# Kernel tuning notes

Measured on AMD Instinct MI355X. Metric: run time of the kernel, lower is better.

The kernel has to match this reference:

```python
import jax, jax.numpy as jnp
import numpy as np

B, N_IN, D_IN = 2048, 49, 320
D = 768            # inner_dim
H = 8              # n_heads
DH = D // H        # head dim = 96
NQ = 8             # n_queries
D_OUT = 3072       # llama_hidden
EPS = 1e-5


def _ln(x, g, b):
    mu = jnp.mean(x, axis=-1, keepdims=True)
    var = jnp.mean(jnp.square(x - mu), axis=-1, keepdims=True)
    return (x - mu) * jax.lax.rsqrt(var + EPS) * g + b


def setup_inputs() -> dict:
    key = jax.random.key(0)
    ks = jax.random.split(key, 16)
    s = lambda k, shape, fan: jax.random.normal(k, shape, jnp.float32) * (1.0 / np.sqrt(fan))
    return {
        "features": jax.random.normal(ks[0], (B, N_IN, D_IN), jnp.float32),
        "input_proj_w": s(ks[1], (D, D_IN), D_IN),
        "input_proj_b": jnp.zeros((D,), jnp.float32),
        "queries": jax.random.normal(ks[2], (NQ, D), jnp.float32) * 0.02,
        "ln_q_g": jnp.ones((D,), jnp.float32), "ln_q_b": jnp.zeros((D,), jnp.float32),
        "ln_kv_g": jnp.ones((D,), jnp.float32), "ln_kv_b": jnp.zeros((D,), jnp.float32),
        "in_proj_w": s(ks[3], (3 * D, D), D),
        "in_proj_b": jnp.zeros((3 * D,), jnp.float32),
        "out_proj_w": s(ks[4], (D, D), D),
        "out_proj_b": jnp.zeros((D,), jnp.float32),
        "ln_ff_g": jnp.ones((D,), jnp.float32), "ln_ff_b": jnp.zeros((D,), jnp.float32),
        "ffn_w1": s(ks[5], (D, D), D), "ffn_b1": jnp.zeros((D,), jnp.float32),
        "ffn_w2": s(ks[6], (D, D), D), "ffn_b2": jnp.zeros((D,), jnp.float32),
        "output_proj_w": s(ks[7], (D_OUT, D), D),
        "output_proj_b": jnp.zeros((D_OUT,), jnp.float32),
        "final_g": jnp.ones((D_OUT,), jnp.float32), "final_b": jnp.zeros((D_OUT,), jnp.float32),
    }


def reference(features, input_proj_w, input_proj_b, queries,
              ln_q_g, ln_q_b, ln_kv_g, ln_kv_b,
              in_proj_w, in_proj_b, out_proj_w, out_proj_b,
              ln_ff_g, ln_ff_b, ffn_w1, ffn_b1, ffn_w2, ffn_b2,
              output_proj_w, output_proj_b, final_g, final_b):
    b = features.shape[0]
    # kv projection: (B, N_in, D)
    kv = jnp.einsum('bnd,ed->bne', features, input_proj_w) + input_proj_b
    q = jnp.broadcast_to(queries[None], (b, NQ, D))

    # --- single layer (n_layers=1) ---
    q_norm = _ln(q, ln_q_g, ln_q_b)
    kv_norm = _ln(kv, ln_kv_g, ln_kv_b)

    wq, wk, wv = in_proj_w[:D], in_proj_w[D:2 * D], in_proj_w[2 * D:]
    bq, bk, bv = in_proj_b[:D], in_proj_b[D:2 * D], in_proj_b[2 * D:]
    qp = (jnp.einsum('bqd,ed->bqe', q_norm, wq) + bq).reshape(b, NQ, H, DH)
    kp = (jnp.einsum('bnd,ed->bne', kv_norm, wk) + bk).reshape(b, N_IN, H, DH)
    vp = (jnp.einsum('bnd,ed->bne', kv_norm, wv) + bv).reshape(b, N_IN, H, DH)

    scores = jnp.einsum('bqhd,bnhd->bhqn', qp, kp) / np.sqrt(DH).astype(np.float32)
    attn = jax.nn.softmax(scores, axis=-1)
    ctx = jnp.einsum('bhqn,bnhd->bqhd', attn, vp).reshape(b, NQ, D)
    attn_out = jnp.einsum('bqd,ed->bqe', ctx, out_proj_w) + out_proj_b

    q = q + attn_out
    h = _ln(q, ln_ff_g, ln_ff_b)
    h = jnp.einsum('bqd,ed->bqe', h, ffn_w1) + ffn_b1
    h = jax.nn.gelu(h, approximate=False)
    h = jnp.einsum('bqd,ed->bqe', h, ffn_w2) + ffn_b2
    q = q + h

    out = jnp.einsum('bqd,ed->bqe', q, output_proj_w) + output_proj_b
    return _ln(out, final_g, final_b)
```

## Files before the change

kernel.cpp:

```cpp
#include <hip/hip_runtime.h>
#include <math.h>

typedef __attribute__((ext_vector_type(8))) short short8;
typedef __attribute__((ext_vector_type(8))) unsigned short ushort8;
typedef __attribute__((ext_vector_type(4))) float f32x4;

__device__ __forceinline__ float b2f(unsigned short h) {
    union { unsigned int u; float f; } c; c.u = ((unsigned int)h) << 16; return c.f;
}
__device__ __forceinline__ unsigned short f2b(float x) {
    union { float f; unsigned int u; } c; c.f = x;
    unsigned int r = c.u + 0x7fffu + ((c.u >> 16) & 1u);
    return (unsigned short)(r >> 16);
}

__global__ __launch_bounds__(256) void cast_f2b(const float* __restrict__ in,
                                                unsigned short* __restrict__ out, int n4) {
    int i = blockIdx.x * 256 + threadIdx.x;
    if (i >= n4) return;
    float4 f = ((const float4*)in)[i];
    ushort4 o; o.x = f2b(f.x); o.y = f2b(f.y); o.z = f2b(f.z); o.w = f2b(f.w);
    ((ushort4*)out)[i] = o;
}

template <int DD, bool INB, bool OUTB>
__global__ __launch_bounds__(256) void ln_rows(const void* __restrict__ in_, void* __restrict__ out_,
                                               const float* __restrict__ g, const float* __restrict__ bb,
                                               int nrows) {
    const int wv = threadIdx.x >> 6, l = threadIdx.x & 63;
    const int row = blockIdx.x * 4 + wv;
    if (row >= nrows) return;
    constexpr int NC = DD / 256;
    float v[DD / 64];
    if constexpr (INB) {
        const ushort4* in = (const ushort4*)((const unsigned short*)in_ + (size_t)row * DD);
#pragma unroll
        for (int c = 0; c < NC; ++c) {
            ushort4 u = in[l + 64 * c];
            v[4*c] = b2f(u.x); v[4*c+1] = b2f(u.y); v[4*c+2] = b2f(u.z); v[4*c+3] = b2f(u.w);
        }
    } else {
        const float4* in = (const float4*)((const float*)in_ + (size_t)row * DD);
#pragma unroll
        for (int c = 0; c < NC; ++c) {
            float4 u = in[l + 64 * c];
            v[4*c] = u.x; v[4*c+1] = u.y; v[4*c+2] = u.z; v[4*c+3] = u.w;
        }
    }
    float s = 0.f, s2 = 0.f;
#pragma unroll
    for (int i = 0; i < DD / 64; ++i) { s += v[i]; s2 += v[i] * v[i]; }
#pragma unroll
    for (int o = 32; o > 0; o >>= 1) { s += __shfl_xor(s, o, 64); s2 += __shfl_xor(s2, o, 64); }
    const float mu = s * (1.0f / DD);
    const float var = s2 * (1.0f / DD) - mu * mu;
    const float rs = rsqrtf(var + 1e-5f);
    if constexpr (OUTB) {
        ushort4* out = (ushort4*)((unsigned short*)out_ + (size_t)row * DD);
#pragma unroll
        for (int c = 0; c < NC; ++c) {
            int e = (l + 64 * c) * 4;
            ushort4 o4;
            o4.x = f2b((v[4*c]   - mu) * rs * g[e]   + bb[e]);
            o4.y = f2b((v[4*c+1] - mu) * rs * g[e+1] + bb[e+1]);
            o4.z = f2b((v[4*c+2] - mu) * rs * g[e+2] + bb[e+2]);
            o4.w = f2b((v[4*c+3] - mu) * rs * g[e+3] + bb[e+3]);
            out[l + 64 * c] = o4;
        }
    } else {
        float4* out = (float4*)((float*)out_ + (size_t)row * DD);
#pragma unroll
        for (int c = 0; c < NC; ++c) {
            int e = (l + 64 * c) * 4;
            float4 o4;
            o4.x = (v[4*c]   - mu) * rs * g[e]   + bb[e];
            o4.y = (v[4*c+1] - mu) * rs * g[e+1] + bb[e+1];
            o4.z = (v[4*c+2] - mu) * rs * g[e+2] + bb[e+2];
            o4.w = (v[4*c+3] - mu) * rs * g[e+3] + bb[e+3];
            out[l + 64 * c] = o4;
        }
    }
}

__global__ __launch_bounds__(256) void ln_stats(const unsigned short* __restrict__ kv,
                                                float2* __restrict__ stats, int nrows) {
    const int wv = threadIdx.x >> 6, l = threadIdx.x & 63;
    const int row = blockIdx.x * 4 + wv;
    if (row >= nrows) return;
    const ushort4* in = (const ushort4*)(kv + (size_t)row * 768);
    float s = 0.f, s2 = 0.f;
#pragma unroll
    for (int c = 0; c < 3; ++c) {
        ushort4 u = in[l + 64 * c];
        float a = b2f(u.x), b = b2f(u.y), cc = b2f(u.z), d = b2f(u.w);
        s += a + b + cc + d;
        s2 += a * a + b * b + cc * cc + d * d;
    }
#pragma unroll
    for (int o = 32; o > 0; o >>= 1) { s += __shfl_xor(s, o, 64); s2 += __shfl_xor(s2, o, 64); }
    const float mu = s * (1.0f / 768.0f);
    const float var = s2 * (1.0f / 768.0f) - mu * mu;
    const float rs = rsqrtf(var + 1e-5f);
    if (l == 0) stats[row] = make_float2(rs, rs * mu);
}

__global__ __launch_bounds__(256) void qp_kernel(const float* __restrict__ qn, const float* __restrict__ wq,
                                                 const float* __restrict__ bq, float* __restrict__ qp) {
    int q = blockIdx.x / 3;
    int col = (blockIdx.x % 3) * 256 + threadIdx.x;
    const float4* a = (const float4*)(qn + q * 768);
    const float4* wr = (const float4*)(wq + (size_t)col * 768);
    float s = 0.f;
#pragma unroll 8
    for (int k = 0; k < 192; ++k) {
        float4 xx = a[k], yy = wr[k];
        s += xx.x * yy.x + xx.y * yy.y + xx.z * yy.z + xx.w * yy.w;
    }
    qp[q * 768 + col] = s + bq[col];
}

__global__ __launch_bounds__(256) void qk_build(const float* __restrict__ qp, const float* __restrict__ wk,
                                                const float* __restrict__ g,
                                                unsigned short* __restrict__ qkg, float* __restrict__ tout) {
    __shared__ float red[4];
    const int hq = blockIdx.x, h = hq >> 3, q = hq & 7;
    const int tid = threadIdx.x;
    const float* qv = qp + q * 768 + h * 96;
    float tsum = 0.f;
#pragma unroll
    for (int c = 0; c < 3; ++c) {
        int e = tid + 256 * c;
        float s = 0.f;
        for (int d = 0; d < 96; ++d) s += qv[d] * wk[(size_t)(h * 96 + d) * 768 + e];
        unsigned short bv = f2b(s * 0.10206207262f * g[e]);
        qkg[hq * 768 + e] = bv;
        tsum += b2f(bv);
    }
#pragma unroll
    for (int o = 32; o > 0; o >>= 1) tsum += __shfl_xor(tsum, o, 64);
    if ((tid & 63) == 0) red[tid >> 6] = tsum;
    __syncthreads();
    if (tid == 0) tout[hq] = red[0] + red[1] + red[2] + red[3];
}

__device__ __forceinline__ void gll16(const void* g, void* l) {
    __builtin_amdgcn_global_load_lds((const __attribute__((address_space(1))) unsigned int*)g,
                                     (__attribute__((address_space(3))) unsigned int*)l, 16, 0, 0);
}

template <int ROWS>
__device__ __forceinline__ void stage_rows(const unsigned short* gbase, int ldg,
                                           unsigned short* lds, int tid) {
    int wuni = tid & ~63;
#pragma unroll
    for (int it = 0; it < ROWS / 32; ++it) {
        int s = it * 256 + tid;
        int r = s >> 3, c = s & 7;
        int cc = c ^ (r & 7);
        gll16(gbase + (size_t)r * ldg + cc * 8, lds + (size_t)(it * 256 + wuni) * 8);
    }
}

template <int EPI>
__global__ __launch_bounds__(256) void gemm_bf16(
    const unsigned short* __restrict__ A, const unsigned short* __restrict__ W,
    const float* __restrict__ bias, void* __restrict__ out,
    const float* __restrict__ aux, int K, int N) {
    __shared__ __align__(16) unsigned short lA[128 * 64];
    __shared__ __align__(16) unsigned short lB[128 * 64];
    const int tid = threadIdx.x;
    const int l = tid & 63, w = tid >> 6;
    int gx = gridDim.x;
    int lid = blockIdx.y * gx + blockIdx.x;
    int nwg = gx * gridDim.y;
    int idx = (nwg & 7) ? lid : ((lid & 7) * (nwg >> 3) + (lid >> 3));
    const int bm0 = (idx / gx) * 128, bn0 = (idx % gx) * 128;
    const int wm = (w >> 1) * 64, wn = (w & 1) * 64;
    const int l15 = l & 15, lk = l >> 4;
    f32x4 acc[4][4] = {};
    const int nk = K >> 6;
    const unsigned short* Abase = A + (size_t)bm0 * K;
    const unsigned short* Wbase = W + (size_t)bn0 * K;
    for (int kt = 0; kt < nk; ++kt) {
        stage_rows<128>(Abase + kt * 64, K, lA, tid);
        stage_rows<128>(Wbase + kt * 64, K, lB, tid);
        __syncthreads();
        short8 af[4], bf[4];
#pragma unroll
        for (int kk = 0; kk < 2; ++kk) {
#pragma unroll
            for (int mf = 0; mf < 4; ++mf) {
                int r = wm + mf * 16 + l15;
                int c = (kk * 4 + lk) ^ (r & 7);
                af[mf] = *(const short8*)(lA + r * 64 + c * 8);
            }
#pragma unroll
            for (int nf = 0; nf < 4; ++nf) {
                int r = wn + nf * 16 + l15;
                int c = (kk * 4 + lk) ^ (r & 7);
                bf[nf] = *(const short8*)(lB + r * 64 + c * 8);
            }
#pragma unroll
            for (int mf = 0; mf < 4; ++mf)
#pragma unroll
                for (int nf = 0; nf < 4; ++nf)
                    acc[mf][nf] = __builtin_amdgcn_mfma_f32_16x16x32_bf16(af[mf], bf[nf], acc[mf][nf], 0, 0, 0);
        }
        __syncthreads();
    }
    const int row0 = bm0 + wm + (lk << 2);
    const int col0 = bn0 + wn + l15;
#pragma unroll
    for (int nf = 0; nf < 4; ++nf) {
        int col = col0 + nf * 16;
        float bv = bias[col];
#pragma unroll
        for (int mf = 0; mf < 4; ++mf) {
#pragma unroll
            for (int r = 0; r < 4; ++r) {
                int row = row0 + mf * 16 + r;
                float v = acc[mf][nf][r] + bv;
                size_t idx2 = (size_t)row * N + col;
                if constexpr (EPI == 0) {
                    ((unsigned short*)out)[idx2] = f2b(v);
                } else if constexpr (EPI == 1) {
                    v += aux[(row & 7) * N + col];
                    ((float*)out)[idx2] = v;
                } else if constexpr (EPI == 2) {
                    v = 0.5f * v * (1.0f + erff(v * 0.70710678118f));
                    ((unsigned short*)out)[idx2] = f2b(v);
                } else if constexpr (EPI == 3) {
                    v += aux[idx2];
                    ((unsigned short*)out)[idx2] = f2b(v);
                } else {
                    ((float*)out)[idx2] = v;
                }
            }
        }
    }
}

__global__ __launch_bounds__(256) void gemm_scores(const unsigned short* __restrict__ A,
                                                   const unsigned short* __restrict__ Qk,
                                                   const float2* __restrict__ stats,
                                                   const float* __restrict__ tcol,
                                                   float* __restrict__ S) {
    __shared__ __align__(16) unsigned short lA[128 * 64];
    __shared__ __align__(16) unsigned short lB[64 * 64];
    const int tid = threadIdx.x;
    const int l = tid & 63, w = tid >> 6;
    int lid = blockIdx.x;
    int idx = (lid & 7) * (gridDim.x >> 3) + (lid >> 3);
    const int bm0 = idx * 128;
    const int wm = (w >> 1) * 64, wn = (w & 1) * 32;
    const int l15 = l & 15, lk = l >> 4;
    f32x4 acc[4][2] = {};
    const unsigned short* Abase = A + (size_t)bm0 * 768;
    for (int kt = 0; kt < 12; ++kt) {
        stage_rows<128>(Abase + kt * 64, 768, lA, tid);
        stage_rows<64>(Qk + kt * 64, 768, lB, tid);
        __syncthreads();
        short8 af[4], bf[2];
#pragma unroll
        for (int kk = 0; kk < 2; ++kk) {
#pragma unroll
            for (int mf = 0; mf < 4; ++mf) {
                int r = wm + mf * 16 + l15;
                int c = (kk * 4 + lk) ^ (r & 7);
                af[mf] = *(const short8*)(lA + r * 64 + c * 8);
            }
#pragma unroll
            for (int nf = 0; nf < 2; ++nf) {
                int r = wn + nf * 16 + l15;
                int c = (kk * 4 + lk) ^ (r & 7);
                bf[nf] = *(const short8*)(lB + r * 64 + c * 8);
            }
#pragma unroll
            for (int mf = 0; mf < 4; ++mf)
#pragma unroll
                for (int nf = 0; nf < 2; ++nf)
                    acc[mf][nf] = __builtin_amdgcn_mfma_f32_16x16x32_bf16(af[mf], bf[nf], acc[mf][nf], 0, 0, 0);
        }
        __syncthreads();
    }
    const int row0 = bm0 + wm + (lk << 2);
    const int col0 = wn + l15;
    const float tv0 = tcol[col0], tv1 = tcol[col0 + 16];
#pragma unroll
    for (int mf = 0; mf < 4; ++mf)
#pragma unroll
        for (int r = 0; r < 4; ++r) {
            int row = row0 + mf * 16 + r;
            float2 st = stats[row];
            S[(size_t)row * 64 + col0]      = st.x * acc[mf][0][r] - st.y * tv0;
            S[(size_t)row * 64 + col0 + 16] = st.x * acc[mf][1][r] - st.y * tv1;
        }
}

__global__ __launch_bounds__(256) void attn_mix(const unsigned short* __restrict__ kvr,
                                                const float* __restrict__ S,
                                                const float2* __restrict__ stats,
                                                const float* __restrict__ lg,
                                                const float* __restrict__ lb,
                                                unsigned short* __restrict__ cmix) {
    __shared__ __align__(16) unsigned short at[64 * 64];
    __shared__ __align__(16) unsigned short kvT[384 * 64];
    __shared__ float dl[64];
    float* Sl = (float*)kvT;
    const int b = blockIdx.x;
    const int t = threadIdx.x, l = t & 63, w = t >> 6;
    const int l15 = l & 15, lk = l >> 4;

    for (int i = t; i < 3136; i += 256) Sl[i] = S[(size_t)b * 3136 + i];
    __syncthreads();
    if (w == 0) {
        float mx = -1e30f;
        for (int n = 0; n < 49; ++n) mx = fmaxf(mx, Sl[n * 64 + l]);
        float sum = 0.f;
        for (int n = 0; n < 49; ++n) sum += __expf(Sl[n * 64 + l] - mx);
        float inv = 1.0f / sum;
        float dacc = 0.f;
#pragma unroll
        for (int c = 0; c < 8; ++c) {
            int cc = c ^ (l & 7);
            for (int j = 0; j < 8; ++j) {
                int n = c * 8 + j;
                float av = 0.f;
                if (n < 49) {
                    float a = __expf(Sl[n * 64 + l] - mx) * inv;
                    float2 st = stats[(size_t)b * 49 + n];
                    av = a * st.x;
                    dacc += a * st.y;
                }
                at[l * 64 + cc * 8 + j] = f2b(av);
            }
        }
        dl[l] = dacc;
    }
    __syncthreads();

    const unsigned short* src = kvr + ((size_t)b * 49 + (l < 49 ? l : 0)) * 768;
#pragma unroll 1
    for (int half = 0; half < 2; ++half) {
        for (int i = 0; i < 12; ++i) {
            int e0 = w * 8 + i * 32;
            ushort8 v = {0, 0, 0, 0, 0, 0, 0, 0};
            if (l < 49) v = *(const ushort8*)(src + half * 384 + e0);
#pragma unroll
            for (int j = 0; j < 8; ++j) {
                int e = e0 + j;
                kvT[e * 64 + (((l >> 3) ^ (e & 7)) << 3) + (l & 7)] = v[j];
            }
        }
        __syncthreads();
#pragma unroll 1
        for (int c2 = 0; c2 < 2; ++c2) {
            int ebase = w * 96 + c2 * 48;
            f32x4 acc[4][3] = {};
#pragma unroll
            for (int ks = 0; ks < 2; ++ks) {
                short8 af[4], bf[3];
#pragma unroll
                for (int mf = 0; mf < 4; ++mf) {
                    int r = mf * 16 + l15;
                    af[mf] = *(const short8*)(at + r * 64 + (((ks * 4 + lk) ^ (r & 7)) << 3));
                }
#pragma unroll
                for (int nf = 0; nf < 3; ++nf) {
                    int er = ebase + nf * 16 + l15;
                    bf[nf] = *(const short8*)(kvT + er * 64 + (((ks * 4 + lk) ^ (er & 7)) << 3));
                }
#pragma unroll
                for (int mf = 0; mf < 4; ++mf)
#pragma unroll
                    for (int nf = 0; nf < 3; ++nf)
                        acc[mf][nf] = __builtin_amdgcn_mfma_f32_16x16x32_bf16(af[mf], bf[nf], acc[mf][nf], 0, 0, 0);
            }
#pragma unroll
            for (int nf = 0; nf < 3; ++nf) {
                int e = half * 384 + ebase + nf * 16 + l15;
                float gg = lg[e], bbv = lb[e];
#pragma unroll
                for (int mf = 0; mf < 4; ++mf)
#pragma unroll
                    for (int r = 0; r < 4; ++r) {
                        int hq = mf * 16 + lk * 4 + r;
                        float val = gg * (acc[mf][nf][r] - dl[hq]) + bbv;
                        cmix[((size_t)(hq >> 3) * 16384 + b * 8 + (hq & 7)) * 768 + e] = f2b(val);
                    }
            }
        }
        __syncthreads();
    }
}

__global__ __launch_bounds__(256) void gemm_ctx(const unsigned short* __restrict__ cmix,
                                                const unsigned short* __restrict__ wvb,
                                                const float* __restrict__ bv,
                                                unsigned short* __restrict__ ctx) {
    __shared__ __align__(16) unsigned short lA[128 * 64];
    __shared__ __align__(16) unsigned short lB[128 * 64];
    const int tid = threadIdx.x;
    const int l = tid & 63, w = tid >> 6;
    const int h = blockIdx.z;
    int yy = blockIdx.y;
    int idx = (yy & 7) * 16 + (yy >> 3);
    const int bm0 = idx * 128;
    const int wm = (w >> 1) * 64, wn = (w & 1) * 64;
    const int l15 = l & 15, lk = l >> 4;
    f32x4 acc[4][4] = {};
    const unsigned short* Abase = cmix + (size_t)h * 16384 * 768 + (size_t)bm0 * 768;
    const unsigned short* Wbase = wvb + (size_t)h * 96 * 768;
    for (int kt = 0; kt < 12; ++kt) {
        stage_rows<128>(Abase + kt * 64, 768, lA, tid);
        stage_rows<128>(Wbase + kt * 64, 768, lB, tid);
        __syncthreads();
        short8 af[4], bf[4];
#pragma unroll
        for (int kk = 0; kk < 2; ++kk) {
#pragma unroll
            for (int mf = 0; mf < 4; ++mf) {
                int r = wm + mf * 16 + l15;
                int c = (kk * 4 + lk) ^ (r & 7);
                af[mf] = *(const short8*)(lA + r * 64 + c * 8);
            }
#pragma unroll
            for (int nf = 0; nf < 4; ++nf) {
                int r = wn + nf * 16 + l15;
                int c = (kk * 4 + lk) ^ (r & 7);
                bf[nf] = *(const short8*)(lB + r * 64 + c * 8);
            }
#pragma unroll
            for (int mf = 0; mf < 4; ++mf)
#pragma unroll
                for (int nf = 0; nf < 4; ++nf)
                    acc[mf][nf] = __builtin_amdgcn_mfma_f32_16x16x32_bf16(af[mf], bf[nf], acc[mf][nf], 0, 0, 0);
        }
        __syncthreads();
    }
    const int row0 = bm0 + wm + (lk << 2);
    const int col0 = wn + l15;
#pragma unroll
    for (int nf = 0; nf < 4; ++nf) {
        int col = col0 + nf * 16;
        if (col >= 96) continue;
        float bvv = bv[h * 96 + col];
#pragma unroll
        for (int mf = 0; mf < 4; ++mf)
#pragma unroll
            for (int r = 0; r < 4; ++r) {
                int row = row0 + mf * 16 + r;
                ctx[(size_t)row * 768 + h * 96 + col] = f2b(acc[mf][nf][r] + bvv);
            }
    }
}

extern "C" void kernel_launch(void* const* d_in, const int* in_sizes, int n_in,
                              void* d_out, int out_size, void* d_ws, size_t ws_size,
                              hipStream_t stream) {
    (void)in_sizes; (void)n_in; (void)out_size;
    const float* features      = (const float*)d_in[0];
    const float* input_proj_w  = (const float*)d_in[1];
    const float* input_proj_b  = (const float*)d_in[2];
    const float* queries       = (const float*)d_in[3];
    const float* ln_q_g        = (const float*)d_in[4];
    const float* ln_q_b        = (const float*)d_in[5];
    const float* ln_kv_g       = (const float*)d_in[6];
    const float* ln_kv_b       = (const float*)d_in[7];
    const float* in_proj_w     = (const float*)d_in[8];
    const float* in_proj_b     = (const float*)d_in[9];
    const float* out_proj_w    = (const float*)d_in[10];
    const float* out_proj_b    = (const float*)d_in[11];
    const float* ln_ff_g       = (const float*)d_in[12];
    const float* ln_ff_b       = (const float*)d_in[13];
    const float* ffn_w1        = (const float*)d_in[14];
    const float* ffn_b1        = (const float*)d_in[15];
    const float* ffn_w2        = (const float*)d_in[16];
    const float* ffn_b2        = (const float*)d_in[17];
    const float* output_proj_w = (const float*)d_in[18];
    const float* output_proj_b = (const float*)d_in[19];
    const float* final_g       = (const float*)d_in[20];
    const float* final_b       = (const float*)d_in[21];

    char* ws = (char*)d_ws;
    size_t off = 0;
    auto alloc = [&](size_t bytes) -> char* {
        char* r = ws + off; off += (bytes + 255) & ~(size_t)255; return r;
    };
    unsigned short* featb = (unsigned short*)alloc(100352ull * 320 * 2);
    unsigned short* kvbuf = (unsigned short*)alloc(100352ull * 768 * 2);
    unsigned short* cmix  = (unsigned short*)alloc(8ull * 16384 * 768 * 2);
    float*          S     = (float*)alloc(100352ull * 64 * 4);
    float2*         stats = (float2*)alloc(100352ull * 8);
    unsigned short* winb  = (unsigned short*)alloc(768ull * 320 * 2);
    unsigned short* wvb   = (unsigned short*)alloc(768ull * 768 * 2);
    unsigned short* woutb = (unsigned short*)alloc(768ull * 768 * 2);
    unsigned short* w1b   = (unsigned short*)alloc(768ull * 768 * 2);
    unsigned short* w2b   = (unsigned short*)alloc(768ull * 768 * 2);
    unsigned short* wopb  = (unsigned short*)alloc(3072ull * 768 * 2);
    float* qnorm          = (float*)alloc(8 * 768 * 4);
    float* qpb            = (float*)alloc(8 * 768 * 4);
    unsigned short* qkb   = (unsigned short*)alloc(64ull * 768 * 2);
    float* tbuf           = (float*)alloc(64 * 4);
    if (off > ws_size) return;

    unsigned short* ctx  = featb;
    unsigned short* outb = kvbuf;
    float* x             = (float*)cmix;
    unsigned short* hn   = (unsigned short*)((char*)cmix + 50331648);
    unsigned short* f1   = (unsigned short*)((char*)cmix + 75497472);
    unsigned short* x2   = (unsigned short*)((char*)cmix + 100663296);

    cast_f2b<<<31360, 256, 0, stream>>>(features, featb, 8028160);
    cast_f2b<<<240,   256, 0, stream>>>(input_proj_w, winb, 61440);
    cast_f2b<<<576,   256, 0, stream>>>(in_proj_w + 2 * 768 * 768, wvb, 147456);
    cast_f2b<<<576,   256, 0, stream>>>(out_proj_w, woutb, 147456);
    cast_f2b<<<576,   256, 0, stream>>>(ffn_w1, w1b, 147456);
    cast_f2b<<<576,   256, 0, stream>>>(ffn_w2, w2b, 147456);
    cast_f2b<<<2304,  256, 0, stream>>>(output_proj_w, wopb, 589824);

    ln_rows<768, false, false><<<2, 256, 0, stream>>>(queries, qnorm, ln_q_g, ln_q_b, 8);
    qp_kernel<<<24, 256, 0, stream>>>(qnorm, in_proj_w, in_proj_b, qpb);
    qk_build<<<64, 256, 0, stream>>>(qpb, in_proj_w + 768 * 768, ln_kv_g, qkb, tbuf);

    gemm_bf16<0><<<dim3(6, 784), 256, 0, stream>>>(featb, winb, input_proj_b, kvbuf, nullptr, 320, 768);
    ln_stats<<<25088, 256, 0, stream>>>(kvbuf, stats, 100352);
    gemm_scores<<<784, 256, 0, stream>>>(kvbuf, qkb, stats, tbuf, S);
    attn_mix<<<2048, 256, 0, stream>>>(kvbuf, S, stats, ln_kv_g, ln_kv_b, cmix);
    gemm_ctx<<<dim3(1, 128, 8), 256, 0, stream>>>(cmix, wvb, in_proj_b + 1536, ctx);
    gemm_bf16<1><<<dim3(6, 128), 256, 0, stream>>>(ctx, woutb, out_proj_b, x, queries, 768, 768);
    ln_rows<768, false, true><<<4096, 256, 0, stream>>>(x, hn, ln_ff_g, ln_ff_b, 16384);
    gemm_bf16<2><<<dim3(6, 128), 256, 0, stream>>>(hn, w1b, ffn_b1, f1, nullptr, 768, 768);
    gemm_bf16<3><<<dim3(6, 128), 256, 0, stream>>>(f1, w2b, ffn_b2, x2, x, 768, 768);
    gemm_bf16<0><<<dim3(24, 128), 256, 0, stream>>>(x2, wopb, output_proj_b, outb, nullptr, 768, 3072);
    ln_rows<3072, true, false><<<4096, 256, 0, stream>>>(outb, (float*)d_out, final_g, final_b, 16384);
}
```

Baseline: 776.3 us.

## Fuse attention mixing with per-head V projection to drop the cmix buffer

```diff
diff --git a/kernel.cpp b/kernel.cpp
--- a/kernel.cpp
+++ b/kernel.cpp
@@ -297,14 +297,17 @@
         }
 }
 
-__global__ __launch_bounds__(256) void attn_mix(const unsigned short* __restrict__ kvr,
+__global__ __launch_bounds__(256) void attn_ctx(const unsigned short* __restrict__ kvr,
                                                 const float* __restrict__ S,
                                                 const float2* __restrict__ stats,
                                                 const float* __restrict__ lg,
                                                 const float* __restrict__ lb,
-                                                unsigned short* __restrict__ cmix) {
+                                                const unsigned short* __restrict__ wvb,
+                                                const float* __restrict__ bv,
+                                                unsigned short* __restrict__ ctx) {
     __shared__ __align__(16) unsigned short at[64 * 64];
-    __shared__ __align__(16) unsigned short kvT[384 * 64];
+    __shared__ __align__(16) unsigned short kvT[192 * 64];
+    __shared__ __align__(16) unsigned short cmixL[64 * 192];
     __shared__ float dl[64];
     float* Sl = (float*)kvT;
     const int b = blockIdx.x;
@@ -339,13 +342,22 @@
     }
     __syncthreads();
 
+    float dlv[4][4];
+#pragma unroll
+    for (int mf = 0; mf < 4; ++mf)
+#pragma unroll
+        for (int r = 0; r < 4; ++r) dlv[mf][r] = dl[mf * 16 + lk * 4 + r];
+
+    f32x4 cacc[12] = {};
     const unsigned short* src = kvr + ((size_t)b * 49 + (l < 49 ? l : 0)) * 768;
+
 #pragma unroll 1
-    for (int half = 0; half < 2; ++half) {
-        for (int i = 0; i < 12; ++i) {
+    for (int ph = 0; ph < 4; ++ph) {
+#pragma unroll
+        for (int i = 0; i < 6; ++i) {
             int e0 = w * 8 + i * 32;
             ushort8 v = {0, 0, 0, 0, 0, 0, 0, 0};
-            if (l < 49) v = *(const ushort8*)(src + half * 384 + e0);
+            if (l < 49) v = *(const ushort8*)(src + ph * 192 + e0);
 #pragma unroll
             for (int j = 0; j < 8; ++j) {
                 int e = e0 + j;
@@ -353,105 +365,82 @@
             }
         }
         __syncthreads();
-#pragma unroll 1
-        for (int c2 = 0; c2 < 2; ++c2) {
-            int ebase = w * 96 + c2 * 48;
-            f32x4 acc[4][3] = {};
-#pragma unroll
-            for (int ks = 0; ks < 2; ++ks) {
-                short8 af[4], bf[3];
-#pragma unroll
-                for (int mf = 0; mf < 4; ++mf) {
-                    int r = mf * 16 + l15;
-                    af[mf] = *(const short8*)(at + r * 64 + (((ks * 4 + lk) ^ (r & 7)) << 3));
+
+        f32x4 macc[4][3] = {};
+#pragma unroll
+        for (int ks = 0; ks < 2; ++ks) {
+            short8 af[4], bf[3];
+#pragma unroll
+            for (int mf = 0; mf < 4; ++mf) {
+                int r = mf * 16 + l15;
+                af[mf] = *(const short8*)(at + r * 64 + (((ks * 4 + lk) ^ (r & 7)) << 3));
+            }
+#pragma unroll
+            for (int nf = 0; nf < 3; ++nf) {
+                int er = w * 48 + nf * 16 + l15;
+                bf[nf] = *(const short8*)(kvT + er * 64 + (((ks * 4 + lk) ^ (er & 7)) << 3));
+            }
+#pragma unroll
+            for (int mf = 0; mf < 4; ++mf)
+#pragma unroll
+                for (int nf = 0; nf < 3; ++nf)
+                    macc[mf][nf] = __builtin_amdgcn_mfma_f32_16x16x32_bf16(af[mf], bf[nf], macc[mf][nf], 0, 0, 0);
+        }
+#pragma unroll
+        for (int nf = 0; nf < 3; ++nf) {
+            int e_local = w * 48 + nf * 16 + l15;
+            int e = ph * 192 + e_local;
+            float gg = lg[e], bbv = lb[e];
+            int c = e_local >> 3;
+#pragma unroll
+            for (int mf = 0; mf < 4; ++mf)
+#pragma unroll
+                for (int r = 0; r < 4; ++r) {
+                    int hq = mf * 16 + lk * 4 + r;
+                    int cs = (c & ~7) | ((c & 7) ^ (hq & 7));
+                    cmixL[hq * 192 + cs * 8 + (e_local & 7)] =
+                        f2b(gg * (macc[mf][nf][r] - dlv[mf][r]) + bbv);
                 }
-#pragma unroll
-                for (int nf = 0; nf < 3; ++nf) {
-                    int er = ebase + nf * 16 + l15;
-                    bf[nf] = *(const short8*)(kvT + er * 64 + (((ks * 4 + lk) ^ (er & 7)) << 3));
+        }
+        __syncthreads();
+
+#pragma unroll
+        for (int jh = 0; jh < 2; ++jh) {
+            int h = w * 2 + jh;
+            int arow = h * 8 + l15;
+            if (arow > 63) arow = 63;
+            short8 af[6];
+#pragma unroll
+            for (int ks = 0; ks < 6; ++ks) {
+                int c = ks * 4 + lk;
+                int cs = (c & ~7) | ((c & 7) ^ (arow & 7));
+                af[ks] = *(const short8*)(cmixL + arow * 192 + cs * 8);
+            }
+#pragma unroll
+            for (int nt = 0; nt < 6; ++nt) {
+                const unsigned short* wp = wvb + (size_t)(h * 96 + nt * 16 + l15) * 768 + ph * 192 + lk * 8;
+#pragma unroll
+                for (int ks = 0; ks < 6; ++ks) {
+                    short8 bf = *(const short8*)(wp + ks * 32);
+                    cacc[jh * 6 + nt] =
+                        __builtin_amdgcn_mfma_f32_16x16x32_bf16(af[ks], bf, cacc[jh * 6 + nt], 0, 0, 0);
                 }
-#pragma unroll
-                for (int mf = 0; mf < 4; ++mf)
-#pragma unroll
-                    for (int nf = 0; nf < 3; ++nf)
-                        acc[mf][nf] = __builtin_amdgcn_mfma_f32_16x16x32_bf16(af[mf], bf[nf], acc[mf][nf], 0, 0, 0);
-            }
-#pragma unroll
-            for (int nf = 0; nf < 3; ++nf) {
-                int e = half * 384 + ebase + nf * 16 + l15;
-                float gg = lg[e], bbv = lb[e];
-#pragma unroll
-                for (int mf = 0; mf < 4; ++mf)
-#pragma unroll
-                    for (int r = 0; r < 4; ++r) {
-                        int hq = mf * 16 + lk * 4 + r;
-                        float val = gg * (acc[mf][nf][r] - dl[hq]) + bbv;
-                        cmix[((size_t)(hq >> 3) * 16384 + b * 8 + (hq & 7)) * 768 + e] = f2b(val);
-                    }
-            }
-        }
-        __syncthreads();
-    }
-}
-
-__global__ __launch_bounds__(256) void gemm_ctx(const unsigned short* __restrict__ cmix,
-                                                const unsigned short* __restrict__ wvb,
-                                                const float* __restrict__ bv,
-                                                unsigned short* __restrict__ ctx) {
-    __shared__ __align__(16) unsigned short lA[128 * 64];
-    __shared__ __align__(16) unsigned short lB[128 * 64];
-    const int tid = threadIdx.x;
-    const int l = tid & 63, w = tid >> 6;
-    const int h = blockIdx.z;
-    int yy = blockIdx.y;
-    int idx = (yy & 7) * 16 + (yy >> 3);
-    const int bm0 = idx * 128;
-    const int wm = (w >> 1) * 64, wn = (w & 1) * 64;
-    const int l15 = l & 15, lk = l >> 4;
-    f32x4 acc[4][4] = {};
-    const unsigned short* Abase = cmix + (size_t)h * 16384 * 768 + (size_t)bm0 * 768;
-    const unsigned short* Wbase = wvb + (size_t)h * 96 * 768;
-    for (int kt = 0; kt < 12; ++kt) {
-        stage_rows<128>(Abase + kt * 64, 768, lA, tid);
-        stage_rows<128>(Wbase + kt * 64, 768, lB, tid);
-        __syncthreads();
-        short8 af[4], bf[4];
-#pragma unroll
-        for (int kk = 0; kk < 2; ++kk) {
-#pragma unroll
-            for (int mf = 0; mf < 4; ++mf) {
-                int r = wm + mf * 16 + l15;
-                int c = (kk * 4 + lk) ^ (r & 7);
-                af[mf] = *(const short8*)(lA + r * 64 + c * 8);
-            }
-#pragma unroll
-            for (int nf = 0; nf < 4; ++nf) {
-                int r = wn + nf * 16 + l15;
-                int c = (kk * 4 + lk) ^ (r & 7);
-                bf[nf] = *(const short8*)(lB + r * 64 + c * 8);
-            }
-#pragma unroll
-            for (int mf = 0; mf < 4; ++mf)
-#pragma unroll
-                for (int nf = 0; nf < 4; ++nf)
-                    acc[mf][nf] = __builtin_amdgcn_mfma_f32_16x16x32_bf16(af[mf], bf[nf], acc[mf][nf], 0, 0, 0);
-        }
-        __syncthreads();
-    }
-    const int row0 = bm0 + wm + (lk << 2);
-    const int col0 = wn + l15;
-#pragma unroll
-    for (int nf = 0; nf < 4; ++nf) {
-        int col = col0 + nf * 16;
-        if (col >= 96) continue;
-        float bvv = bv[h * 96 + col];
-#pragma unroll
-        for (int mf = 0; mf < 4; ++mf)
+            }
+        }
+    }
+
+    if (lk < 2) {
+#pragma unroll
+        for (int j = 0; j < 12; ++j) {
+            int h = w * 2 + j / 6, nt = j % 6;
+            int col = h * 96 + nt * 16 + l15;
+            float bbv = bv[col];
 #pragma unroll
             for (int r = 0; r < 4; ++r) {
-                int row = row0 + mf * 16 + r;
-                ctx[(size_t)row * 768 + h * 96 + col] = f2b(acc[mf][nf][r] + bvv);
-            }
+                int q = lk * 4 + r;
+                ctx[((size_t)b * 8 + q) * 768 + col] = f2b(cacc[j][r] + bbv);
+            }
+        }
     }
 }
 
@@ -489,7 +478,10 @@
     };
     unsigned short* featb = (unsigned short*)alloc(100352ull * 320 * 2);
     unsigned short* kvbuf = (unsigned short*)alloc(100352ull * 768 * 2);
-    unsigned short* cmix  = (unsigned short*)alloc(8ull * 16384 * 768 * 2);
+    float*          x     = (float*)alloc(16384ull * 768 * 4);
+    unsigned short* hn    = (unsigned short*)alloc(16384ull * 768 * 2);
+    unsigned short* f1    = (unsigned short*)alloc(16384ull * 768 * 2);
+    unsigned short* x2    = (unsigned short*)alloc(16384ull * 768 * 2);
     float*          S     = (float*)alloc(100352ull * 64 * 4);
     float2*         stats = (float2*)alloc(100352ull * 8);
     unsigned short* winb  = (unsigned short*)alloc(768ull * 320 * 2);
@@ -506,10 +498,6 @@
 
     unsigned short* ctx  = featb;
     unsigned short* outb = kvbuf;
-    float* x             = (float*)cmix;
-    unsigned short* hn   = (unsigned short*)((char*)cmix + 50331648);
-    unsigned short* f1   = (unsigned short*)((char*)cmix + 75497472);
-    unsigned short* x2   = (unsigned short*)((char*)cmix + 100663296);
 
     cast_f2b<<<31360, 256, 0, stream>>>(features, featb, 8028160);
     cast_f2b<<<240,   256, 0, stream>>>(input_proj_w, winb, 61440);
@@ -526,8 +514,7 @@
     gemm_bf16<0><<<dim3(6, 784), 256, 0, stream>>>(featb, winb, input_proj_b, kvbuf, nullptr, 320, 768);
     ln_stats<<<25088, 256, 0, stream>>>(kvbuf, stats, 100352);
     gemm_scores<<<784, 256, 0, stream>>>(kvbuf, qkb, stats, tbuf, S);
-    attn_mix<<<2048, 256, 0, stream>>>(kvbuf, S, stats, ln_kv_g, ln_kv_b, cmix);
-    gemm_ctx<<<dim3(1, 128, 8), 256, 0, stream>>>(cmix, wvb, in_proj_b + 1536, ctx);
+    attn_ctx<<<2048, 256, 0, stream>>>(kvbuf, S, stats, ln_kv_g, ln_kv_b, wvb, in_proj_b + 1536, ctx);
     gemm_bf16<1><<<dim3(6, 128), 256, 0, stream>>>(ctx, woutb, out_proj_b, x, queries, 768, 768);
     ln_rows<768, false, true><<<4096, 256, 0, stream>>>(x, hn, ln_ff_g, ln_ff_b, 16384);
     gemm_bf16<2><<<dim3(6, 128), 256, 0, stream>>>(hn, w1b, ffn_b1, f1, nullptr, 768, 768);
```

After: 918.6 us. +18.3%, slower.
